# Kernel tuning notes

Hardware: AMD Instinct MI355X
Metric: run time of the kernel (lower is better)

The kernel has to match this reference:

```python
import jax, jax.numpy as jnp
import numpy as np
from jax import lax

T, D, H = 8192, 1024, 1024
FORGET_BIAS = 1.0  # BasicLSTMCell default


def setup_inputs() -> dict:
    key = jax.random.key(0)
    ks = jax.random.split(key, 5)
    x = jax.random.normal(ks[0], (T, D), dtype=jnp.float32)
    c_in = jax.random.normal(ks[1], (1, H), dtype=jnp.float32)
    h_in = jax.random.normal(ks[2], (1, H), dtype=jnp.float32)
    # BasicLSTMCell kernel [D+H, 4H], gates ordered (i, j, f, o); glorot-ish scale
    W_lstm = jax.random.normal(ks[3], (D + H, 4 * H), dtype=jnp.float32) * (1.0 / np.sqrt(D + H))
    b_lstm = jnp.zeros((4 * H,), dtype=jnp.float32)
    # normc_initializer(1.0): columns normalized to unit norm
    W_out = jax.random.normal(ks[4], (H, H), dtype=jnp.float32)
    W_out = W_out / jnp.linalg.norm(W_out, axis=0, keepdims=True)
    b_out = jnp.zeros((H,), dtype=jnp.float32)
    return {"x": x, "c_in": c_in, "h_in": h_in, "W_lstm": W_lstm,
            "b_lstm": b_lstm, "W_out": W_out, "b_out": b_out}


def reference(x, c_in, h_in, W_lstm, b_lstm, W_out, b_out):
    # Precompute the input contribution for all timesteps in one big GEMM;
    # the recurrence only needs the h @ W_h part per step.
    Wx, Wh = W_lstm[:D], W_lstm[D:]          # [D,4H], [H,4H]
    xz = x @ Wx + b_lstm                      # [T, 4H]

    def step(carry, xz_t):
        c, h = carry                          # [H], [H]
        z = xz_t + h @ Wh                     # [4H]
        i, j, f, o = jnp.split(z, 4)
        new_c = c * jax.nn.sigmoid(f + FORGET_BIAS) + jax.nn.sigmoid(i) * jnp.tanh(j)
        new_h = jnp.tanh(new_c) * jax.nn.sigmoid(o)
        return (new_c, new_h), new_h

    (c_last, h_last), hs = lax.scan(step, (c_in[0], h_in[0]), xz)  # hs: [T, H]
    output = hs @ W_out + b_out               # final_layer (no activation)
    return output, c_last[None, :], h_last[None, :]
```

## Files before the change

### kernel.cpp

```cpp
#include <hip/hip_runtime.h>

#define T_STEPS 8192
#define DD 1024
#define HH 1024
#define NWG 256
#define NTHR 512
#define SCOPE_AGENT __HIP_MEMORY_SCOPE_AGENT
typedef unsigned long long u64;

__device__ __forceinline__ int swz(int k) { return k ^ ((((k) >> 6) & 3) << 2); }

__device__ __forceinline__ float fsig(float v) {
  return 1.f / (1.f + __expf(-v));
}
__device__ __forceinline__ float ftanh(float v) {
  return 2.f / (1.f + __expf(-2.f * v)) - 1.f;
}

__global__ __launch_bounds__(NTHR, 1) void lstm_scan(
    const float* __restrict__ x, const float* __restrict__ c_in,
    const float* __restrict__ h_in, const float* __restrict__ W,
    const float* __restrict__ b, float* __restrict__ Hs,
    u64* __restrict__ hbuf,
    float* __restrict__ out_tail)
{
  const int g = blockIdx.x, tid = threadIdx.x;
  const int lane = tid & 63, wave = tid >> 6;
  const int col = tid & 15, seg = tid >> 4;
  const int gate = col >> 2, hi = col & 3;
  const int cg = gate * HH + g * 4 + hi;

  __shared__ float Wl[32768];
  __shared__ float xb[DD];
  __shared__ float hb[HH];
  __shared__ float partial[8][16];

  float c_reg = 0.f, hlast = 0.f;

  if (tid < 4) {
    const float h0 = h_in[g * 4 + tid];
    c_reg = c_in[g * 4 + tid];
    const u64 pv = ((u64)1u << 32) | (u64)__float_as_uint(h0);
    __hip_atomic_store(&hbuf[g * 4 + tid], pv, __ATOMIC_RELAXED, SCOPE_AGENT);
  }

  #pragma unroll
  for (int j = 0; j < 16; ++j) {
    float4 v;
    v.x = W[(size_t)(seg * 64 + j * 4 + 0) * (4 * HH) + cg];
    v.y = W[(size_t)(seg * 64 + j * 4 + 1) * (4 * HH) + cg];
    v.z = W[(size_t)(seg * 64 + j * 4 + 2) * (4 * HH) + cg];
    v.w = W[(size_t)(seg * 64 + j * 4 + 3) * (4 * HH) + cg];
    *(float4*)&Wl[(wave * 16 + j) * 256 + lane * 4] = v;
  }

  const float bias_reg = b[((lane & 15) >> 2) * HH + g * 4 + (lane & 3)];

  float xv0 = x[tid], xv1 = x[tid + 512];

  __syncthreads();

  const bool is_x = (wave < 4);

  for (int t = 1; t <= T_STEPS; ++t) {
    xb[swz(tid)]       = xv0;
    xb[swz(tid + 512)] = xv1;
    __syncthreads();

    if (t < T_STEPS) {
      const float* xn = x + (size_t)t * DD;
      xv0 = xn[tid];
      xv1 = xn[tid + 512];
    }

    if (is_x) {
      float p = 0.f;
      #pragma unroll
      for (int j = 0; j < 16; ++j) {
        const float4 wv = *(const float4*)&Wl[(wave * 16 + j) * 256 + lane * 4];
        const float4 xv = *(const float4*)&xb[(seg * 64 + j * 4) ^ ((seg & 3) << 2)];
        p = fmaf(xv.x, wv.x, p); p = fmaf(xv.y, wv.y, p);
        p = fmaf(xv.z, wv.z, p); p = fmaf(xv.w, wv.w, p);
      }
      p += __shfl_xor(p, 16);
      p += __shfl_xor(p, 32);
      if (lane < 16) partial[wave][lane] = p;
    } else {
      const u64* hp = hbuf + ((t - 1) & 1) * HH;
      const int cb = (wave - 4) * 256;
      const unsigned tg = (unsigned)t;
      u64 a0 = __hip_atomic_load(&hp[cb + lane],       __ATOMIC_RELAXED, SCOPE_AGENT);
      u64 a1 = __hip_atomic_load(&hp[cb + 64 + lane],  __ATOMIC_RELAXED, SCOPE_AGENT);
      u64 a2 = __hip_atomic_load(&hp[cb + 128 + lane], __ATOMIC_RELAXED, SCOPE_AGENT);
      u64 a3 = __hip_atomic_load(&hp[cb + 192 + lane], __ATOMIC_RELAXED, SCOPE_AGENT);
      bool r0 = (unsigned)(a0 >> 32) >= tg;
      bool r1 = (unsigned)(a1 >> 32) >= tg;
      bool r2 = (unsigned)(a2 >> 32) >= tg;
      bool r3 = (unsigned)(a3 >> 32) >= tg;
      while (!(r0 & r1 & r2 & r3)) {
        if (!r0) { a0 = __hip_atomic_load(&hp[cb + lane],       __ATOMIC_RELAXED, SCOPE_AGENT); r0 = (unsigned)(a0 >> 32) >= tg; }
        if (!r1) { a1 = __hip_atomic_load(&hp[cb + 64 + lane],  __ATOMIC_RELAXED, SCOPE_AGENT); r1 = (unsigned)(a1 >> 32) >= tg; }
        if (!r2) { a2 = __hip_atomic_load(&hp[cb + 128 + lane], __ATOMIC_RELAXED, SCOPE_AGENT); r2 = (unsigned)(a2 >> 32) >= tg; }
        if (!r3) { a3 = __hip_atomic_load(&hp[cb + 192 + lane], __ATOMIC_RELAXED, SCOPE_AGENT); r3 = (unsigned)(a3 >> 32) >= tg; }
      }
      hb[swz(cb + lane)]       = __uint_as_float((unsigned)a0);
      hb[swz(cb + 64 + lane)]  = __uint_as_float((unsigned)a1);
      hb[swz(cb + 128 + lane)] = __uint_as_float((unsigned)a2);
      hb[swz(cb + 192 + lane)] = __uint_as_float((unsigned)a3);
      asm volatile("s_waitcnt lgkmcnt(0)" ::: "memory");
      const int s2 = seg - 16;
      float q = 0.f;
      #pragma unroll
      for (int j = 0; j < 16; ++j) {
        const float4 wv = *(const float4*)&Wl[(wave * 16 + j) * 256 + lane * 4];
        const float4 hv = *(const float4*)&hb[(s2 * 64 + j * 4) ^ ((s2 & 3) << 2)];
        q = fmaf(hv.x, wv.x, q); q = fmaf(hv.y, wv.y, q);
        q = fmaf(hv.z, wv.z, q); q = fmaf(hv.w, wv.w, q);
      }
      q += __shfl_xor(q, 16);
      q += __shfl_xor(q, 32);
      if (lane < 16) partial[wave][lane] = q;
    }
    __syncthreads();

    if (wave == 0) {
      float zsum = bias_reg;
      #pragma unroll
      for (int wv = 0; wv < 8; ++wv) zsum += partial[wv][lane & 15];
      const int gt = (lane & 15) >> 2;
      const float zin = (gt == 1) ? (2.f * zsum) : (gt == 2 ? zsum + 1.f : zsum);
      const float s = 1.f / (1.f + __expf(-zin));
      const float act = (gt == 1) ? (2.f * s - 1.f) : s;
      const float ig = __shfl(act, tid);
      const float tj = __shfl(act, tid + 4);
      const float fg = __shfl(act, tid + 8);
      const float og = __shfl(act, tid + 12);
      if (tid < 4) {
        const float nc = c_reg * fg + ig * tj;
        const float nh = ftanh(nc) * og;
        c_reg = nc; hlast = nh;
        const u64 pv = ((u64)(unsigned)(t + 1) << 32) | (u64)__float_as_uint(nh);
        __hip_atomic_store(&hbuf[(t & 1) * HH + g * 4 + tid], pv,
                           __ATOMIC_RELAXED, SCOPE_AGENT);
        Hs[(size_t)(t - 1) * HH + g * 4 + tid] = nh;
      }
    }
  }

  if (tid < 4) {
    out_tail[g * 4 + tid]      = c_reg;
    out_tail[HH + g * 4 + tid] = hlast;
  }
}

#define BM 64
#define BN 64
#define BK 16
__global__ __launch_bounds__(256, 2) void out_gemm(
    const float* __restrict__ A,
    const float* __restrict__ Bw,
    const float* __restrict__ bias,
    float* __restrict__ C)
{
  __shared__ float As[BM][BK];
  __shared__ float Bs[BK][BN];
  const int tid = threadIdx.x;
  const int row0 = blockIdx.y * BM, col0 = blockIdx.x * BN;
  const int tx = tid & 15, ty = tid >> 4;

  float acc[4][4];
  #pragma unroll
  for (int j = 0; j < 4; ++j) {
    const float bv = bias[col0 + tx * 4 + j];
    #pragma unroll
    for (int i = 0; i < 4; ++i) acc[i][j] = bv;
  }

  for (int k0 = 0; k0 < HH; k0 += BK) {
    {
      const int r = tid >> 2, c = (tid & 3) * 4;
      const float4 va = *(const float4*)&A[(size_t)(row0 + r) * HH + k0 + c];
      As[r][c] = va.x; As[r][c + 1] = va.y; As[r][c + 2] = va.z; As[r][c + 3] = va.w;
      const int rb = tid >> 4, cb = (tid & 15) * 4;
      *(float4*)&Bs[rb][cb] = *(const float4*)&Bw[(size_t)(k0 + rb) * HH + col0 + cb];
    }
    __syncthreads();
    #pragma unroll
    for (int kk = 0; kk < BK; ++kk) {
      float a[4], bv[4];
      #pragma unroll
      for (int i = 0; i < 4; ++i) a[i] = As[ty * 4 + i][kk];
      #pragma unroll
      for (int j = 0; j < 4; ++j) bv[j] = Bs[kk][tx * 4 + j];
      #pragma unroll
      for (int i = 0; i < 4; ++i)
        #pragma unroll
        for (int j = 0; j < 4; ++j)
          acc[i][j] = fmaf(a[i], bv[j], acc[i][j]);
    }
    __syncthreads();
  }

  #pragma unroll
  for (int i = 0; i < 4; ++i) {
    float4 v = make_float4(acc[i][0], acc[i][1], acc[i][2], acc[i][3]);
    *(float4*)&C[(size_t)(row0 + ty * 4 + i) * HH + col0 + tx * 4] = v;
  }
}

extern "C" void kernel_launch(void* const* d_in, const int* in_sizes, int n_in,
                              void* d_out, int out_size, void* d_ws, size_t ws_size,
                              hipStream_t stream) {
  const float* x    = (const float*)d_in[0];
  const float* c_in = (const float*)d_in[1];
  const float* h_in = (const float*)d_in[2];
  const float* W    = (const float*)d_in[3];
  const float* b    = (const float*)d_in[4];
  const float* Wout = (const float*)d_in[5];
  const float* bout = (const float*)d_in[6];
  float* out = (float*)d_out;

  u64* hbuf = (u64*)d_ws;
  float* Hs = (float*)(hbuf + 2 * HH);
  float* out_tail = out + (size_t)T_STEPS * HH;

  hipMemsetAsync(hbuf, 0, 2 * HH * sizeof(u64), stream);

  void* args[] = {(void*)&x, (void*)&c_in, (void*)&h_in, (void*)&W, (void*)&b,
                  (void*)&Hs, (void*)&hbuf, (void*)&out_tail};
  hipLaunchCooperativeKernel((void*)lstm_scan, dim3(NWG), dim3(NTHR),
                             args, 0, stream);

  out_gemm<<<dim3(HH / BN, T_STEPS / BM), 256, 0, stream>>>(Hs, Wout, bout, out);
}
```

Measured before the change: 12.97 ms.

## Decouple x-projection waves from recurrence via LDS flags, drop block barriers

Splits the workgroup into producer waves that compute the input projection and run ahead, double-buffered through LDS, and consumer waves that each own one hidden unit and compute the h-projection plus gate math locally. Both __syncthreads per step are replaced with workgroup-scope flag spinning, so the x-projection for step t can overlap the wait on the global h exchange. The W layout is reshuffled so each h-wave covers the full K range for one hidden column across the four gates. This adds intra-workgroup spin loops and relies on relaxed LDS atomics plus waitcnt for ordering, which carries correctness and livelock risk.

```diff
diff --git a/kernel.cpp b/kernel.cpp
--- a/kernel.cpp
+++ b/kernel.cpp
@@ -6,13 +6,9 @@
 #define NWG 256
 #define NTHR 512
 #define SCOPE_AGENT __HIP_MEMORY_SCOPE_AGENT
+#define SCOPE_WG __HIP_MEMORY_SCOPE_WORKGROUP
 typedef unsigned long long u64;
 
-__device__ __forceinline__ int swz(int k) { return k ^ ((((k) >> 6) & 3) << 2); }
-
-__device__ __forceinline__ float fsig(float v) {
-  return 1.f / (1.f + __expf(-v));
-}
 __device__ __forceinline__ float ftanh(float v) {
   return 2.f / (1.f + __expf(-2.f * v)) - 1.f;
 }
@@ -26,68 +22,107 @@
 {
   const int g = blockIdx.x, tid = threadIdx.x;
   const int lane = tid & 63, wave = tid >> 6;
-  const int col = tid & 15, seg = tid >> 4;
-  const int gate = col >> 2, hi = col & 3;
-  const int cg = gate * HH + g * 4 + hi;
+  const bool is_x = (wave < 4);
 
   __shared__ float Wl[32768];
-  __shared__ float xb[DD];
-  __shared__ float hb[HH];
-  __shared__ float partial[8][16];
-
-  float c_reg = 0.f, hlast = 0.f;
+  __shared__ float xc[4][256];
+  __shared__ float hb[2][1024];
+  __shared__ float xpart[2][4][16];
+  __shared__ int xflag[2][4];
+  __shared__ int cflag[2][4];
+  __shared__ int xdone[2][4];
 
   if (tid < 4) {
+    xflag[0][tid] = 0; xflag[1][tid] = 0;
+    cflag[0][tid] = 0; cflag[1][tid] = 0;
+    xdone[0][tid] = 0; xdone[1][tid] = 0;
     const float h0 = h_in[g * 4 + tid];
-    c_reg = c_in[g * 4 + tid];
     const u64 pv = ((u64)1u << 32) | (u64)__float_as_uint(h0);
     __hip_atomic_store(&hbuf[g * 4 + tid], pv, __ATOMIC_RELAXED, SCOPE_AGENT);
   }
 
-  #pragma unroll
-  for (int j = 0; j < 16; ++j) {
-    float4 v;
-    v.x = W[(size_t)(seg * 64 + j * 4 + 0) * (4 * HH) + cg];
-    v.y = W[(size_t)(seg * 64 + j * 4 + 1) * (4 * HH) + cg];
-    v.z = W[(size_t)(seg * 64 + j * 4 + 2) * (4 * HH) + cg];
-    v.w = W[(size_t)(seg * 64 + j * 4 + 3) * (4 * HH) + cg];
-    *(float4*)&Wl[(wave * 16 + j) * 256 + lane * 4] = v;
-  }
-
-  const float bias_reg = b[((lane & 15) >> 2) * HH + g * 4 + (lane & 3)];
-
-  float xv0 = x[tid], xv1 = x[tid + 512];
+  if (is_x) {
+    const int col = lane & 15, sseg = lane >> 4;
+    const int cgx = (col >> 2) * HH + g * 4 + (col & 3);
+    #pragma unroll
+    for (int j = 0; j < 16; ++j) {
+      float4 v;
+      v.x = W[(size_t)(wave * 256 + sseg * 64 + j * 4 + 0) * (4 * HH) + cgx];
+      v.y = W[(size_t)(wave * 256 + sseg * 64 + j * 4 + 1) * (4 * HH) + cgx];
+      v.z = W[(size_t)(wave * 256 + sseg * 64 + j * 4 + 2) * (4 * HH) + cgx];
+      v.w = W[(size_t)(wave * 256 + sseg * 64 + j * 4 + 3) * (4 * HH) + cgx];
+      *(float4*)&Wl[wave * 4096 + j * 256 + lane * 4] = v;
+    }
+  } else {
+    const int e = wave - 4, gate = lane & 3, kseg = lane >> 2;
+    const int cgh = gate * HH + g * 4 + e;
+    #pragma unroll
+    for (int j = 0; j < 16; ++j) {
+      float4 v;
+      v.x = W[(size_t)(DD + kseg * 64 + j * 4 + 0) * (4 * HH) + cgh];
+      v.y = W[(size_t)(DD + kseg * 64 + j * 4 + 1) * (4 * HH) + cgh];
+      v.z = W[(size_t)(DD + kseg * 64 + j * 4 + 2) * (4 * HH) + cgh];
+      v.w = W[(size_t)(DD + kseg * 64 + j * 4 + 3) * (4 * HH) + cgh];
+      *(float4*)&Wl[wave * 4096 + j * 256 + lane * 4] = v;
+    }
+  }
+
+  float c_reg = 0.f, hlast = 0.f, bias_l = 0.f;
+  if (!is_x) {
+    bias_l = b[(lane & 3) * HH + g * 4 + (wave - 4)];
+    c_reg = c_in[g * 4 + (wave - 4)];
+  }
+
+  float4 xv = make_float4(0.f, 0.f, 0.f, 0.f);
+  if (is_x) xv = *(const float4*)&x[wave * 256 + lane * 4];
 
   __syncthreads();
 
-  const bool is_x = (wave < 4);
-
-  for (int t = 1; t <= T_STEPS; ++t) {
-    xb[swz(tid)]       = xv0;
-    xb[swz(tid + 512)] = xv1;
-    __syncthreads();
-
-    if (t < T_STEPS) {
-      const float* xn = x + (size_t)t * DD;
-      xv0 = xn[tid];
-      xv1 = xn[tid + 512];
-    }
-
-    if (is_x) {
-      float p = 0.f;
+  if (is_x) {
+    const int sseg = lane >> 4;
+    const int sswz = (sseg & 3) << 2;
+    for (int t = 1; t <= T_STEPS; ++t) {
+      const int p = t & 1;
+      *(float4*)&xc[wave][(lane * 4) ^ sswz] = xv;
+      if (t < T_STEPS)
+        xv = *(const float4*)&x[(size_t)t * DD + wave * 256 + lane * 4];
+      asm volatile("s_waitcnt lgkmcnt(0)" ::: "memory");
+      float pa = 0.f;
       #pragma unroll
       for (int j = 0; j < 16; ++j) {
-        const float4 wv = *(const float4*)&Wl[(wave * 16 + j) * 256 + lane * 4];
-        const float4 xv = *(const float4*)&xb[(seg * 64 + j * 4) ^ ((seg & 3) << 2)];
-        p = fmaf(xv.x, wv.x, p); p = fmaf(xv.y, wv.y, p);
-        p = fmaf(xv.z, wv.z, p); p = fmaf(xv.w, wv.w, p);
-      }
-      p += __shfl_xor(p, 16);
-      p += __shfl_xor(p, 32);
-      if (lane < 16) partial[wave][lane] = p;
-    } else {
+        const float4 wv = *(const float4*)&Wl[wave * 4096 + j * 256 + lane * 4];
+        const float4 xq = *(const float4*)&xc[wave][(sseg * 64 + j * 4) ^ sswz];
+        pa = fmaf(xq.x, wv.x, pa); pa = fmaf(xq.y, wv.y, pa);
+        pa = fmaf(xq.z, wv.z, pa); pa = fmaf(xq.w, wv.w, pa);
+      }
+      pa += __shfl_xor(pa, 16);
+      pa += __shfl_xor(pa, 32);
+      {
+        const int tm2 = t - 2;
+        for (;;) {
+          const int d0 = __hip_atomic_load(&xdone[p][0], __ATOMIC_RELAXED, SCOPE_WG);
+          const int d1 = __hip_atomic_load(&xdone[p][1], __ATOMIC_RELAXED, SCOPE_WG);
+          const int d2 = __hip_atomic_load(&xdone[p][2], __ATOMIC_RELAXED, SCOPE_WG);
+          const int d3 = __hip_atomic_load(&xdone[p][3], __ATOMIC_RELAXED, SCOPE_WG);
+          if (d0 >= tm2 && d1 >= tm2 && d2 >= tm2 && d3 >= tm2) break;
+          __builtin_amdgcn_s_sleep(1);
+        }
+      }
+      asm volatile("" ::: "memory");
+      if (lane < 16) xpart[p][wave][lane] = pa;
+      asm volatile("s_waitcnt lgkmcnt(0)" ::: "memory");
+      if (lane == 0)
+        __hip_atomic_store(&xflag[p][wave], t, __ATOMIC_RELAXED, SCOPE_WG);
+    }
+  } else {
+    const int e = wave - 4;
+    const int gate = lane & 3, kseg = lane >> 2;
+    const int kswz = (kseg & 3) << 2;
+    const int cb = e * 256;
+    const int colw = gate * 4 + e;
+    for (int t = 1; t <= T_STEPS; ++t) {
+      const int p = t & 1;
       const u64* hp = hbuf + ((t - 1) & 1) * HH;
-      const int cb = (wave - 4) * 256;
       const unsigned tg = (unsigned)t;
       u64 a0 = __hip_atomic_load(&hp[cb + lane],       __ATOMIC_RELAXED, SCOPE_AGENT);
       u64 a1 = __hip_atomic_load(&hp[cb + 64 + lane],  __ATOMIC_RELAXED, SCOPE_AGENT);
@@ -103,53 +138,65 @@
         if (!r2) { a2 = __hip_atomic_load(&hp[cb + 128 + lane], __ATOMIC_RELAXED, SCOPE_AGENT); r2 = (unsigned)(a2 >> 32) >= tg; }
         if (!r3) { a3 = __hip_atomic_load(&hp[cb + 192 + lane], __ATOMIC_RELAXED, SCOPE_AGENT); r3 = (unsigned)(a3 >> 32) >= tg; }
       }
-      hb[swz(cb + lane)]       = __uint_as_float((unsigned)a0);
-      hb[swz(cb + 64 + lane)]  = __uint_as_float((unsigned)a1);
-      hb[swz(cb + 128 + lane)] = __uint_as_float((unsigned)a2);
-      hb[swz(cb + 192 + lane)] = __uint_as_float((unsigned)a3);
-      asm volatile("s_waitcnt lgkmcnt(0)" ::: "memory");
-      const int s2 = seg - 16;
+      hb[p][(cb + lane)]            = __uint_as_float((unsigned)a0);
+      hb[p][(cb + 64 + lane) ^ 4]   = __uint_as_float((unsigned)a1);
+      hb[p][(cb + 128 + lane) ^ 8]  = __uint_as_float((unsigned)a2);
+      hb[p][(cb + 192 + lane) ^ 12] = __uint_as_float((unsigned)a3);
+      asm volatile("s_waitcnt lgkmcnt(0)" ::: "memory");
+      if (lane == 0)
+        __hip_atomic_store(&cflag[p][e], t, __ATOMIC_RELAXED, SCOPE_WG);
+      for (;;) {
+        const int c0 = __hip_atomic_load(&cflag[p][0], __ATOMIC_RELAXED, SCOPE_WG);
+        const int c1 = __hip_atomic_load(&cflag[p][1], __ATOMIC_RELAXED, SCOPE_WG);
+        const int c2 = __hip_atomic_load(&cflag[p][2], __ATOMIC_RELAXED, SCOPE_WG);
+        const int c3 = __hip_atomic_load(&cflag[p][3], __ATOMIC_RELAXED, SCOPE_WG);
+        const int f0 = __hip_atomic_load(&xflag[p][0], __ATOMIC_RELAXED, SCOPE_WG);
+        const int f1 = __hip_atomic_load(&xflag[p][1], __ATOMIC_RELAXED, SCOPE_WG);
+        const int f2 = __hip_atomic_load(&xflag[p][2], __ATOMIC_RELAXED, SCOPE_WG);
+        const int f3 = __hip_atomic_load(&xflag[p][3], __ATOMIC_RELAXED, SCOPE_WG);
+        if (c0 >= t && c1 >= t && c2 >= t && c3 >= t &&
+            f0 >= t && f1 >= t && f2 >= t && f3 >= t) break;
+      }
+      asm volatile("" ::: "memory");
       float q = 0.f;
       #pragma unroll
       for (int j = 0; j < 16; ++j) {
-        const float4 wv = *(const float4*)&Wl[(wave * 16 + j) * 256 + lane * 4];
-        const float4 hv = *(const float4*)&hb[(s2 * 64 + j * 4) ^ ((s2 & 3) << 2)];
+        const float4 wv = *(const float4*)&Wl[wave * 4096 + j * 256 + lane * 4];
+        const float4 hv = *(const float4*)&hb[p][(kseg * 64 + j * 4) ^ kswz];
         q = fmaf(hv.x, wv.x, q); q = fmaf(hv.y, wv.y, q);
         q = fmaf(hv.z, wv.z, q); q = fmaf(hv.w, wv.w, q);
       }
+      q += __shfl_xor(q, 4);
+      q += __shfl_xor(q, 8);
       q += __shfl_xor(q, 16);
       q += __shfl_xor(q, 32);
-      if (lane < 16) partial[wave][lane] = q;
-    }
-    __syncthreads();
-
-    if (wave == 0) {
-      float zsum = bias_reg;
-      #pragma unroll
-      for (int wv = 0; wv < 8; ++wv) zsum += partial[wv][lane & 15];
-      const int gt = (lane & 15) >> 2;
-      const float zin = (gt == 1) ? (2.f * zsum) : (gt == 2 ? zsum + 1.f : zsum);
+      const float z = bias_l + q +
+                      xpart[p][0][colw] + xpart[p][1][colw] +
+                      xpart[p][2][colw] + xpart[p][3][colw];
+      const float zin = (gate == 1) ? (2.f * z) : (gate == 2 ? z + 1.f : z);
       const float s = 1.f / (1.f + __expf(-zin));
-      const float act = (gt == 1) ? (2.f * s - 1.f) : s;
-      const float ig = __shfl(act, tid);
-      const float tj = __shfl(act, tid + 4);
-      const float fg = __shfl(act, tid + 8);
-      const float og = __shfl(act, tid + 12);
-      if (tid < 4) {
-        const float nc = c_reg * fg + ig * tj;
-        const float nh = ftanh(nc) * og;
-        c_reg = nc; hlast = nh;
+      const float act = (gate == 1) ? (2.f * s - 1.f) : s;
+      const float ig = __shfl(act, 0);
+      const float tj = __shfl(act, 1);
+      const float fg = __shfl(act, 2);
+      const float og = __shfl(act, 3);
+      const float nc = c_reg * fg + ig * tj;
+      const float nh = ftanh(nc) * og;
+      c_reg = nc; hlast = nh;
+      if (lane == 0) {
         const u64 pv = ((u64)(unsigned)(t + 1) << 32) | (u64)__float_as_uint(nh);
-        __hip_atomic_store(&hbuf[(t & 1) * HH + g * 4 + tid], pv,
+        __hip_atomic_store(&hbuf[(t & 1) * HH + g * 4 + e], pv,
                            __ATOMIC_RELAXED, SCOPE_AGENT);
-        Hs[(size_t)(t - 1) * HH + g * 4 + tid] = nh;
-      }
-    }
-  }
-
-  if (tid < 4) {
-    out_tail[g * 4 + tid]      = c_reg;
-    out_tail[HH + g * 4 + tid] = hlast;
+        Hs[(size_t)(t - 1) * HH + g * 4 + e] = nh;
+      }
+      asm volatile("s_waitcnt lgkmcnt(0)" ::: "memory");
+      if (lane == 0)
+        __hip_atomic_store(&xdone[p][e], t, __ATOMIC_RELAXED, SCOPE_WG);
+    }
+    if (lane == 0) {
+      out_tail[g * 4 + e]      = c_reg;
+      out_tail[HH + g * 4 + e] = hlast;
+    }
   }
 }
 
```

Result: slower. 37.84 ms (+191.6%).

## Enlarge output GEMM tiles to 128x128 with 8x8 register blocking

Applied to the files above, without the earlier changes.

The output projection GEMM now uses 128x128 block tiles with an 8x8 per-thread micro-tile instead of 64x64 and 4x4. A is stored transposed and padded in shared memory, and B uses a swizzled, padded layout, so each thread reads its inputs with float4 LDS loads. The goal is more FMAs per shared-memory load and per global byte, which should shorten the GEMM phase. The cost is higher register pressure, since 64 accumulators per thread may limit occupancy, and fewer blocks in the grid. The recurrent scan, which probably dominates total time, is unchanged.

```diff
diff --git a/kernel.cpp b/kernel.cpp
--- a/kernel.cpp
+++ b/kernel.cpp
@@ -153,58 +153,74 @@
   }
 }
 
-#define BM 64
-#define BN 64
+#define BM 128
+#define BN 128
 #define BK 16
+__device__ __forceinline__ int bswz(int c) { return c ^ (((c >> 5) & 1) << 2); }
+
 __global__ __launch_bounds__(256, 2) void out_gemm(
     const float* __restrict__ A,
     const float* __restrict__ Bw,
     const float* __restrict__ bias,
     float* __restrict__ C)
 {
-  __shared__ float As[BM][BK];
-  __shared__ float Bs[BK][BN];
+  __shared__ float As[BK][BM + 4];
+  __shared__ float Bs[BK][BN + 4];
   const int tid = threadIdx.x;
   const int row0 = blockIdx.y * BM, col0 = blockIdx.x * BN;
   const int tx = tid & 15, ty = tid >> 4;
 
-  float acc[4][4];
+  const int ar = tid >> 1;
+  const int ac = (tid & 1) * 8;
+  const int br = tid >> 4;
+  const int bc = (tid & 15) * 8;
+
+  float acc[8][8];
   #pragma unroll
-  for (int j = 0; j < 4; ++j) {
-    const float bv = bias[col0 + tx * 4 + j];
+  for (int i = 0; i < 8; ++i)
     #pragma unroll
-    for (int i = 0; i < 4; ++i) acc[i][j] = bv;
-  }
+    for (int j = 0; j < 8; ++j) acc[i][j] = 0.f;
 
   for (int k0 = 0; k0 < HH; k0 += BK) {
-    {
-      const int r = tid >> 2, c = (tid & 3) * 4;
-      const float4 va = *(const float4*)&A[(size_t)(row0 + r) * HH + k0 + c];
-      As[r][c] = va.x; As[r][c + 1] = va.y; As[r][c + 2] = va.z; As[r][c + 3] = va.w;
-      const int rb = tid >> 4, cb = (tid & 15) * 4;
-      *(float4*)&Bs[rb][cb] = *(const float4*)&Bw[(size_t)(k0 + rb) * HH + col0 + cb];
-    }
+    const float4 a0 = *(const float4*)&A[(size_t)(row0 + ar) * HH + k0 + ac];
+    const float4 a1 = *(const float4*)&A[(size_t)(row0 + ar) * HH + k0 + ac + 4];
+    const float4 b0 = *(const float4*)&Bw[(size_t)(k0 + br) * HH + col0 + bc];
+    const float4 b1 = *(const float4*)&Bw[(size_t)(k0 + br) * HH + col0 + bc + 4];
+    As[ac + 0][ar] = a0.x; As[ac + 1][ar] = a0.y;
+    As[ac + 2][ar] = a0.z; As[ac + 3][ar] = a0.w;
+    As[ac + 4][ar] = a1.x; As[ac + 5][ar] = a1.y;
+    As[ac + 6][ar] = a1.z; As[ac + 7][ar] = a1.w;
+    *(float4*)&Bs[br][bswz(bc)]     = b0;
+    *(float4*)&Bs[br][bswz(bc + 4)] = b1;
     __syncthreads();
     #pragma unroll
     for (int kk = 0; kk < BK; ++kk) {
-      float a[4], bv[4];
-      #pragma unroll
-      for (int i = 0; i < 4; ++i) a[i] = As[ty * 4 + i][kk];
-      #pragma unroll
-      for (int j = 0; j < 4; ++j) bv[j] = Bs[kk][tx * 4 + j];
-      #pragma unroll
-      for (int i = 0; i < 4; ++i)
+      float a[8], bb[8];
+      *(float4*)&a[0]  = *(const float4*)&As[kk][ty * 8];
+      *(float4*)&a[4]  = *(const float4*)&As[kk][ty * 8 + 4];
+      *(float4*)&bb[0] = *(const float4*)&Bs[kk][bswz(tx * 8)];
+      *(float4*)&bb[4] = *(const float4*)&Bs[kk][bswz(tx * 8 + 4)];
+      #pragma unroll
+      for (int i = 0; i < 8; ++i)
         #pragma unroll
-        for (int j = 0; j < 4; ++j)
-          acc[i][j] = fmaf(a[i], bv[j], acc[i][j]);
+        for (int j = 0; j < 8; ++j)
+          acc[i][j] = fmaf(a[i], bb[j], acc[i][j]);
     }
     __syncthreads();
   }
 
   #pragma unroll
-  for (int i = 0; i < 4; ++i) {
-    float4 v = make_float4(acc[i][0], acc[i][1], acc[i][2], acc[i][3]);
-    *(float4*)&C[(size_t)(row0 + ty * 4 + i) * HH + col0 + tx * 4] = v;
+  for (int i = 0; i < 8; ++i) {
+    const size_t r = (size_t)(row0 + ty * 8 + i) * HH;
+    #pragma unroll
+    for (int j = 0; j < 8; j += 4) {
+      float4 v;
+      v.x = acc[i][j + 0] + bias[col0 + tx * 8 + j + 0];
+      v.y = acc[i][j + 1] + bias[col0 + tx * 8 + j + 1];
+      v.z = acc[i][j + 2] + bias[col0 + tx * 8 + j + 2];
+      v.w = acc[i][j + 3] + bias[col0 + tx * 8 + j + 3];
+      *(float4*)&C[r + col0 + tx * 8 + j] = v;
+    }
   }
 }
 
```

New measurement: 12.99 ms, median of 2. No clear change (+0.1%).
